# Kernel optimization log

Hardware: AMD Instinct MI355X
Metric: run time of the kernel (lower is better)

Reference implementation:

```python
import jax, jax.numpy as jnp
import numpy as np

NUM_HEADS = 4
NUM_GROUPS = 8
EPS = 1e-5


def group_norm(x, gamma, beta):
    # x: [b, c, h, w], GroupNorm with NUM_GROUPS groups, eps=1e-5
    b, c, h, w = x.shape
    xg = x.reshape(b, NUM_GROUPS, (c // NUM_GROUPS) * h * w)
    mean = jnp.mean(xg, axis=-1, keepdims=True)
    var = jnp.var(xg, axis=-1, keepdims=True)
    xn = ((xg - mean) * jax.lax.rsqrt(var + EPS)).reshape(b, c, h, w)
    return xn * gamma[None, :, None, None] + beta[None, :, None, None]


def setup_inputs() -> dict:
    key = jax.random.key(0)
    ks = jax.random.split(key, 4)
    b, c, h, w = 4, 256, 64, 64
    x = jax.random.normal(ks[0], (b, c, h, w), dtype=jnp.float32)
    gamma = jnp.ones((c,), dtype=jnp.float32)
    beta = jnp.zeros((c,), dtype=jnp.float32)
    w_qkv = jax.random.normal(ks[1], (3 * c, c), dtype=jnp.float32) * (c ** -0.5)
    b_qkv = jnp.zeros((3 * c,), dtype=jnp.float32)
    w_proj = jax.random.normal(ks[2], (c, c), dtype=jnp.float32) * (c ** -0.5)
    b_proj = jnp.zeros((c,), dtype=jnp.float32)
    return {"x": x, "gamma": gamma, "beta": beta, "w_qkv": w_qkv,
            "b_qkv": b_qkv, "w_proj": w_proj, "b_proj": b_proj}


def reference(x, gamma, beta, w_qkv, b_qkv, w_proj, b_proj):
    b, c, h, w = x.shape
    heads = NUM_HEADS
    dim = c // heads
    n = h * w
    residual = x
    xn = group_norm(x, gamma, beta)
    # 1x1 conv == per-pixel linear: [b,c,h,w] x [3c,c] -> [b,3c,h,w]
    qkv = jnp.einsum('bchw,oc->bohw', xn, w_qkv) + b_qkv[None, :, None, None]
    # channel layout: (three, heads, dim)
    qkv = qkv.reshape(b, 3, heads, dim, n)            # [b,3,H,D,N]
    qkv = jnp.transpose(qkv, (1, 0, 2, 4, 3))         # [3,b,H,N,D]
    q, k, v = qkv[0], qkv[1], qkv[2]
    scale = dim ** -0.5
    scores = jnp.einsum('bhid,bhjd->bhij', q * scale, k)  # [b,H,N,N]
    attn = jax.nn.softmax(scores, axis=-1)
    out = jnp.einsum('bhij,bhjd->bhid', attn, v)          # [b,H,N,D]
    out = jnp.transpose(out, (0, 1, 3, 2)).reshape(b, c, h, w)
    out = jnp.einsum('bchw,oc->bohw', out, w_proj) + b_proj[None, :, None, None]
    return out + residual
```

## Files before the change

### kernel.cpp

```cpp
#include <hip/hip_runtime.h>
#include <stdint.h>

typedef unsigned short ushort_t;
typedef __attribute__((ext_vector_type(8))) short bf16x8;
typedef __attribute__((ext_vector_type(4))) float f32x4;
typedef __attribute__((ext_vector_type(16))) float f32x16;
typedef __attribute__((ext_vector_type(4))) unsigned int u32x4;

__device__ __forceinline__ ushort_t f2bf(float f) {
  union { float f; unsigned u; } v; v.f = f;
  unsigned r = v.u + 0x7fffu + ((v.u >> 16) & 1u);
  return (ushort_t)(r >> 16);
}
__device__ __forceinline__ unsigned bfbits(float f) {
  union { float f; unsigned u; } v; v.f = f; return v.u;
}
__device__ __forceinline__ unsigned pack_trunc(float lo, float hi) {
#if __has_builtin(__builtin_amdgcn_perm)
  return __builtin_amdgcn_perm(bfbits(hi), bfbits(lo), 0x07060302u);
#else
  return (bfbits(lo) >> 16) | (bfbits(hi) & 0xffff0000u);
#endif
}
__device__ __forceinline__ unsigned pack_rn(float lo, float hi) {
  return (unsigned)f2bf(lo) | ((unsigned)f2bf(hi) << 16);
}
__device__ __forceinline__ void swap32(unsigned &a, unsigned &b) {
#if __has_builtin(__builtin_amdgcn_permlane32_swap)
  auto r = __builtin_amdgcn_permlane32_swap(a, b, false, false);
  a = r[0]; b = r[1];
#else
  asm volatile("v_permlane32_swap_b32 %0, %1" : "+v"(a), "+v"(b));
#endif
}
__device__ __forceinline__ float fast_exp2(float x) {
#if __has_builtin(__builtin_amdgcn_exp2f)
  return __builtin_amdgcn_exp2f(x);
#else
  float r; asm("v_exp_f32 %0, %1" : "=v"(r) : "v"(x)); return r;
#endif
}

#define SCALE_Q 0.18033688011112042f
#define EXP_BIAS 23.083109273961734f

__global__ __launch_bounds__(256)
void gn_stats1(const float* __restrict__ x, float2* __restrict__ partial) {
  int blk = blockIdx.x, tid = threadIdx.x;
  const float* base = x + (size_t)blk * 16384;
  float s = 0.f, ss = 0.f;
  for (int i = tid * 4; i < 16384; i += 1024) {
    float4 v = *(const float4*)(base + i);
    s  += v.x + v.y + v.z + v.w;
    ss += v.x*v.x + v.y*v.y + v.z*v.z + v.w*v.w;
  }
  __shared__ float rs[256], rss[256];
  rs[tid] = s; rss[tid] = ss;
  __syncthreads();
  for (int off = 128; off > 0; off >>= 1) {
    if (tid < off) { rs[tid] += rs[tid+off]; rss[tid] += rss[tid+off]; }
    __syncthreads();
  }
  if (tid == 0) partial[blk] = make_float2(rs[0], rss[0]);
}

__global__ __launch_bounds__(64)
void gn_stats2(const float2* __restrict__ partial, float* __restrict__ stats) {
  int g = threadIdx.x;
  if (g < 32) {
    float s = 0.f, ss = 0.f;
    #pragma unroll
    for (int k = 0; k < 8; k++) { float2 p = partial[g*8 + k]; s += p.x; ss += p.y; }
    float mean = s * (1.f/131072.f);
    float var  = ss * (1.f/131072.f) - mean*mean;
    stats[g*2]   = mean;
    stats[g*2+1] = rsqrtf(var + 1e-5f);
  }
}

__global__ __launch_bounds__(256)
void gn_apply_t(const float* __restrict__ x, const float* __restrict__ stats,
                const float* __restrict__ gamma, const float* __restrict__ beta,
                ushort_t* __restrict__ xn_t, int b0) {
  int blk = blockIdx.x;
  int tid = threadIdx.x;
  int ct = blk & 7;
  int nt = (blk >> 3) & 15;
  int bl = blk >> 7;
  int b  = b0 + bl;
  int c0 = ct * 32;
  float mean = stats[(b*8 + ct)*2];
  float rstd = stats[(b*8 + ct)*2 + 1];
  __shared__ ushort_t Ls[32][264];
  for (int idx = tid; idx < 32*64; idx += 256) {
    int cc = idx >> 6, seg = idx & 63;
    float ga = gamma[c0+cc], be = beta[c0+cc];
    float a = rstd * ga;
    float bb = be - mean * a;
    float4 v = *(const float4*)(x + ((size_t)(b*256 + c0 + cc))*4096 + nt*256 + seg*4);
    ushort4 t4 = make_ushort4(f2bf(v.x*a+bb), f2bf(v.y*a+bb), f2bf(v.z*a+bb), f2bf(v.w*a+bb));
    *(ushort4*)&Ls[cc][seg*4] = t4;
  }
  __syncthreads();
  for (int idx = tid; idx < 256*4; idx += 256) {
    int n = idx >> 2, seg = idx & 3;
    union { ushort_t u[8]; uint4 v; } pk;
    #pragma unroll
    for (int e = 0; e < 8; e++) pk.u[e] = Ls[seg*8 + e][n];
    *(uint4*)(xn_t + ((size_t)(bl*4096 + nt*256 + n))*256 + c0 + seg*8) = pk.v;
  }
}

__global__ __launch_bounds__(256)
void wconv2(const float* __restrict__ wq, const float* __restrict__ wp,
            ushort_t* __restrict__ oq, ushort_t* __restrict__ op) {
  int blk = blockIdx.x;
  const float* w; ushort_t* o; int i;
  if (blk < 192) { w = wq; o = oq; i = blk*256 + threadIdx.x; }
  else           { w = wp; o = op; i = (blk-192)*256 + threadIdx.x; }
  float4 v = *(const float4*)(w + (size_t)i*4);
  *(ushort4*)(o + (size_t)i*4) = make_ushort4(f2bf(v.x), f2bf(v.y), f2bf(v.z), f2bf(v.w));
}

__global__ __launch_bounds__(256)
void gemm_qkv(const ushort_t* __restrict__ A, const ushort_t* __restrict__ Bt,
              const float* __restrict__ bias, ushort_t* __restrict__ q,
              ushort_t* __restrict__ kbuf, ushort_t* __restrict__ vt, int b0) {
  int blk = blockIdx.x;
  int nt = blk % 12, mt = blk / 12;
  int m0 = mt*128, n0 = nt*64;
  int tid = threadIdx.x;
  int wave = tid >> 6, lane = tid & 63, quad = lane >> 4, l16 = lane & 15;
  __shared__ ushort_t As[128][40];
  __shared__ ushort_t Bs[64][40];
  __shared__ ushort_t Lt[64][136];
  f32x4 acc[2][4];
  #pragma unroll
  for (int i = 0; i < 2; i++)
    #pragma unroll
    for (int j = 0; j < 4; j++) acc[i][j] = (f32x4){0.f,0.f,0.f,0.f};

  for (int k0 = 0; k0 < 256; k0 += 32) {
    #pragma unroll
    for (int i = tid; i < 512; i += 256) {
      int row = i >> 2, seg = i & 3;
      *(uint4*)&As[row][seg*8] = *(const uint4*)(A + (size_t)(m0+row)*256 + k0 + seg*8);
    }
    {
      int row = tid >> 2, seg = tid & 3;
      *(uint4*)&Bs[row][seg*8] = *(const uint4*)(Bt + (size_t)(n0+row)*256 + k0 + seg*8);
    }
    __syncthreads();
    bf16x8 af[2], bfr[4];
    #pragma unroll
    for (int t = 0; t < 2; t++) af[t]  = *(const bf16x8*)&As[wave*32 + t*16 + l16][quad*8];
    #pragma unroll
    for (int t = 0; t < 4; t++) bfr[t] = *(const bf16x8*)&Bs[t*16 + l16][quad*8];
    #pragma unroll
    for (int ti = 0; ti < 2; ti++)
      #pragma unroll
      for (int jn = 0; jn < 4; jn++)
        acc[ti][jn] = __builtin_amdgcn_mfma_f32_16x16x32_bf16(af[ti], bfr[jn], acc[ti][jn], 0, 0, 0);
    __syncthreads();
  }

  int region = nt >> 2;
  if (region == 0) {
    #pragma unroll
    for (int jn = 0; jn < 4; jn++) {
      int n = n0 + jn*16 + l16;
      float bv = bias[n];
      #pragma unroll
      for (int ti = 0; ti < 2; ti++) {
        int mrow = m0 + wave*32 + ti*16 + quad*4;
        #pragma unroll
        for (int r = 0; r < 4; r++)
          q[(size_t)(b0*4096 + mrow + r)*256 + n] = f2bf((acc[ti][jn][r] + bv) * SCALE_Q);
      }
    }
  } else if (region == 1) {
    #pragma unroll
    for (int jn = 0; jn < 4; jn++) {
      int n = n0 + jn*16 + l16;
      float bv = bias[n];
      #pragma unroll
      for (int ti = 0; ti < 2; ti++) {
        int mrow = m0 + wave*32 + ti*16 + quad*4;
        #pragma unroll
        for (int r = 0; r < 4; r++)
          kbuf[(size_t)(b0*4096 + mrow + r)*256 + (n - 256)] = f2bf(acc[ti][jn][r] + bv);
      }
    }
  } else {
    int hh = nt - 8;
    int b_loc = m0 >> 12;
    #pragma unroll
    for (int jn = 0; jn < 4; jn++) {
      int n = n0 + jn*16 + l16;
      float bv = bias[n];
      int drow = jn*16 + l16;
      #pragma unroll
      for (int ti = 0; ti < 2; ti++) {
        int tcol = wave*32 + ti*16 + quad*4;
        uint2 w;
        w.x = pack_rn(acc[ti][jn][0] + bv, acc[ti][jn][1] + bv);
        w.y = pack_rn(acc[ti][jn][2] + bv, acc[ti][jn][3] + bv);
        *(uint2*)&Lt[drow][tcol] = w;
      }
    }
    __syncthreads();
    size_t vb_ = ((size_t)((b0 + b_loc)*4 + hh)*64)*4096 + (size_t)(m0 & 4095);
    for (int idx = tid; idx < 1024; idx += 256) {
      int dd = idx >> 4, toff = (idx & 15)*8;
      *(uint4*)(vt + vb_ + (size_t)dd*4096 + toff) = *(const uint4*)&Lt[dd][toff];
    }
  }
}

__global__ __launch_bounds__(256)
void attn(ushort_t* __restrict__ q, const ushort_t* __restrict__ k,
          const ushort_t* __restrict__ vt, int cpx) {
  int L = blockIdx.x;
  int blk = (L & 7) * cpx + (L >> 3);
  int it = blk & 31;
  int h  = (blk >> 5) & 3;
  int b  = blk >> 7;
  int i0 = it * 128;
  int tid = threadIdx.x;
  int wave = tid >> 6, lane = tid & 63;
  int q32 = lane & 31, hi = lane >> 5;

  __shared__ ushort_t Ks[2][64][72];
  __shared__ ushort_t Vs[2][64][72];

  const ushort_t* kbase = k + (size_t)(b*4096)*256 + h*64;
  const ushort_t* vbase = vt + (size_t)(b*4 + h)*64*4096;
  ushort_t* qrow = q + (size_t)(b*4096 + i0 + wave*32 + q32)*256 + h*64;

  bf16x8 qb0 = *(const bf16x8*)(qrow      + hi*8);
  bf16x8 qb1 = *(const bf16x8*)(qrow + 16 + hi*8);
  bf16x8 qb2 = *(const bf16x8*)(qrow + 32 + hi*8);
  bf16x8 qb3 = *(const bf16x8*)(qrow + 48 + hi*8);

  bf16x8 ones;
  #pragma unroll
  for (int e = 0; e < 8; e++) ones[e] = (short)0x3F80;

  f32x16 bias_init;
  #pragma unroll
  for (int r = 0; r < 16; r++) bias_init[r] = -EXP_BIAS;

  f32x16 o_acc0, o_acc1, l_acc;
  #pragma unroll
  for (int r = 0; r < 16; r++) { o_acc0[r] = 0.f; o_acc1[r] = 0.f; l_acc[r] = 0.f; }

  int srow = tid >> 2, scol = (tid & 3) * 16;
  const ushort_t* kp = kbase + (size_t)srow*256 + scol;
  const ushort_t* vp = vbase + (size_t)srow*4096 + scol;
  uint4 rk0, rk1, rv0, rv1;
  #define LOADK() { \
    rk0 = *(const uint4*)(kp); \
    rk1 = *(const uint4*)(kp + 8); \
    kp += 64*256; }
  #define WRITEK(BI) { \
    *(uint4*)&Ks[BI][srow][scol]     = rk0; \
    *(uint4*)&Ks[BI][srow][scol + 8] = rk1; }
  #define LOADV() { \
    rv0 = *(const uint4*)(vp); \
    rv1 = *(const uint4*)(vp + 8); \
    vp += 64; }
  #define WRITEV(BI) { \
    *(uint4*)&Vs[BI][srow][scol]     = rv0; \
    *(uint4*)&Vs[BI][srow][scol + 8] = rv1; }

  #define SOFTMAX(S, PB0, PB1) \
    _Pragma("unroll") \
    for (int r = 0; r < 16; r++) S[r] = fast_exp2(S[r]); \
    { unsigned pkA = pack_trunc(S[0],  S[1]),  pkB = pack_trunc(S[2],  S[3]); \
      unsigned pkC = pack_trunc(S[4],  S[5]),  pkD = pack_trunc(S[6],  S[7]); \
      unsigned pkE = pack_trunc(S[8],  S[9]),  pkF = pack_trunc(S[10], S[11]); \
      unsigned pkG = pack_trunc(S[12], S[13]), pkH = pack_trunc(S[14], S[15]); \
      swap32(pkA, pkC); swap32(pkB, pkD); \
      swap32(pkE, pkG); swap32(pkF, pkH); \
      u32x4 w0_ = {pkA, pkB, pkC, pkD}; \
      u32x4 w1_ = {pkE, pkF, pkG, pkH}; \
      PB0 = __builtin_bit_cast(bf16x8, w0_); \
      PB1 = __builtin_bit_cast(bf16x8, w1_); }

  #define WINDOW(BI) { \
    bf16x8 k00 = *(const bf16x8*)&Ks[BI][q32     ][hi*8]; \
    bf16x8 k01 = *(const bf16x8*)&Ks[BI][q32     ][16 + hi*8]; \
    bf16x8 k02 = *(const bf16x8*)&Ks[BI][q32     ][32 + hi*8]; \
    bf16x8 k03 = *(const bf16x8*)&Ks[BI][q32     ][48 + hi*8]; \
    bf16x8 k10 = *(const bf16x8*)&Ks[BI][32 + q32][hi*8]; \
    bf16x8 k11 = *(const bf16x8*)&Ks[BI][32 + q32][16 + hi*8]; \
    bf16x8 k12 = *(const bf16x8*)&Ks[BI][32 + q32][32 + hi*8]; \
    bf16x8 k13 = *(const bf16x8*)&Ks[BI][32 + q32][48 + hi*8]; \
    __builtin_amdgcn_s_setprio(1); \
    f32x16 s0 = __builtin_amdgcn_mfma_f32_32x32x16_bf16(k00, qb0, bias_init, 0, 0, 0); \
    s0 = __builtin_amdgcn_mfma_f32_32x32x16_bf16(k01, qb1, s0, 0, 0, 0); \
    s0 = __builtin_amdgcn_mfma_f32_32x32x16_bf16(k02, qb2, s0, 0, 0, 0); \
    s0 = __builtin_amdgcn_mfma_f32_32x32x16_bf16(k03, qb3, s0, 0, 0, 0); \
    f32x16 s1 = __builtin_amdgcn_mfma_f32_32x32x16_bf16(k10, qb0, bias_init, 0, 0, 0); \
    s1 = __builtin_amdgcn_mfma_f32_32x32x16_bf16(k11, qb1, s1, 0, 0, 0); \
    s1 = __builtin_amdgcn_mfma_f32_32x32x16_bf16(k12, qb2, s1, 0, 0, 0); \
    s1 = __builtin_amdgcn_mfma_f32_32x32x16_bf16(k13, qb3, s1, 0, 0, 0); \
    bf16x8 pb00, pb01, pb10, pb11; \
    SOFTMAX(s0, pb00, pb01)    \
    { bf16x8 vb00 = *(const bf16x8*)&Vs[BI][q32     ][hi*8]; \
      bf16x8 vb01 = *(const bf16x8*)&Vs[BI][q32     ][16 + hi*8]; \
      bf16x8 vb10 = *(const bf16x8*)&Vs[BI][32 + q32][hi*8]; \
      bf16x8 vb11 = *(const bf16x8*)&Vs[BI][32 + q32][16 + hi*8]; \
      o_acc0 = __builtin_amdgcn_mfma_f32_32x32x16_bf16(vb00, pb00, o_acc0, 0, 0, 0); \
      o_acc0 = __builtin_amdgcn_mfma_f32_32x32x16_bf16(vb01, pb01, o_acc0, 0, 0, 0); \
      o_acc1 = __builtin_amdgcn_mfma_f32_32x32x16_bf16(vb10, pb00, o_acc1, 0, 0, 0); \
      o_acc1 = __builtin_amdgcn_mfma_f32_32x32x16_bf16(vb11, pb01, o_acc1, 0, 0, 0); \
      l_acc  = __builtin_amdgcn_mfma_f32_32x32x16_bf16(ones, pb00, l_acc, 0, 0, 0); \
      l_acc  = __builtin_amdgcn_mfma_f32_32x32x16_bf16(ones, pb01, l_acc, 0, 0, 0); } \
    SOFTMAX(s1, pb10, pb11)    \
    { bf16x8 vb00 = *(const bf16x8*)&Vs[BI][q32     ][32 + hi*8]; \
      bf16x8 vb01 = *(const bf16x8*)&Vs[BI][q32     ][48 + hi*8]; \
      bf16x8 vb10 = *(const bf16x8*)&Vs[BI][32 + q32][32 + hi*8]; \
      bf16x8 vb11 = *(const bf16x8*)&Vs[BI][32 + q32][48 + hi*8]; \
      o_acc0 = __builtin_amdgcn_mfma_f32_32x32x16_bf16(vb00, pb10, o_acc0, 0, 0, 0); \
      o_acc0 = __builtin_amdgcn_mfma_f32_32x32x16_bf16(vb01, pb11, o_acc0, 0, 0, 0); \
      o_acc1 = __builtin_amdgcn_mfma_f32_32x32x16_bf16(vb10, pb10, o_acc1, 0, 0, 0); \
      o_acc1 = __builtin_amdgcn_mfma_f32_32x32x16_bf16(vb11, pb11, o_acc1, 0, 0, 0); \
      l_acc  = __builtin_amdgcn_mfma_f32_32x32x16_bf16(ones, pb10, l_acc, 0, 0, 0); \
      l_acc  = __builtin_amdgcn_mfma_f32_32x32x16_bf16(ones, pb11, l_acc, 0, 0, 0); } \
    __builtin_amdgcn_s_setprio(0); \
  }

  LOADK(); LOADV(); WRITEK(0); WRITEV(0);
  __syncthreads();

  #pragma unroll 2
  for (int w = 0; w < 64; w++) {
    int cur = w & 1;
    if (w < 63) { LOADK(); LOADV(); }
    WINDOW(cur)
    if (w < 63) { WRITEK(cur ^ 1); WRITEV(cur ^ 1); }
    __syncthreads();
  }
  #undef LOADK
  #undef LOADV
  #undef WRITEK
  #undef WRITEV
  #undef WINDOW
  #undef SOFTMAX

  float inv = 1.f / l_acc[0];

  #pragma unroll
  for (int g = 0; g < 4; g++) {
    ushort4 u;
    u.x = f2bf(o_acc0[g*4+0]*inv); u.y = f2bf(o_acc0[g*4+1]*inv);
    u.z = f2bf(o_acc0[g*4+2]*inv); u.w = f2bf(o_acc0[g*4+3]*inv);
    *(ushort4*)(qrow + g*8 + hi*4) = u;
  }
  #pragma unroll
  for (int g = 0; g < 4; g++) {
    ushort4 u;
    u.x = f2bf(o_acc1[g*4+0]*inv); u.y = f2bf(o_acc1[g*4+1]*inv);
    u.z = f2bf(o_acc1[g*4+2]*inv); u.w = f2bf(o_acc1[g*4+3]*inv);
    *(ushort4*)(qrow + 32 + g*8 + hi*4) = u;
  }
}

__global__ __launch_bounds__(256)
void gemm_proj(const ushort_t* __restrict__ A,
               const ushort_t* __restrict__ Bt,
               const float* __restrict__ bias, const float* __restrict__ resid,
               float* __restrict__ out, int col_base) {
  int blk = blockIdx.x;
  int mt = blk & 1, nt = blk >> 1;
  int m0 = mt*128, n0 = nt*64;
  int tid = threadIdx.x;
  int wave = tid >> 6, lane = tid & 63, quad = lane >> 4, l16 = lane & 15;
  __shared__ ushort_t As[128][40];
  __shared__ ushort_t Bs[64][40];
  f32x4 acc[2][4];
  #pragma unroll
  for (int i = 0; i < 2; i++)
    #pragma unroll
    for (int j = 0; j < 4; j++) acc[i][j] = (f32x4){0.f,0.f,0.f,0.f};

  for (int k0 = 0; k0 < 256; k0 += 32) {
    #pragma unroll
    for (int i = tid; i < 512; i += 256) {
      int row = i >> 2, seg = i & 3;
      *(uint4*)&As[row][seg*8] = *(const uint4*)(A + (size_t)(m0+row)*256 + k0 + seg*8);
    }
    {
      int row = tid >> 2, seg = tid & 3;
      *(uint4*)&Bs[row][seg*8] = *(const uint4*)(Bt + (size_t)(n0+row)*256 + k0 + seg*8);
    }
    __syncthreads();
    bf16x8 af[2], bfr[4];
    #pragma unroll
    for (int t = 0; t < 2; t++) af[t]  = *(const bf16x8*)&As[wave*32 + t*16 + l16][quad*8];
    #pragma unroll
    for (int t = 0; t < 4; t++) bfr[t] = *(const bf16x8*)&Bs[t*16 + l16][quad*8];
    #pragma unroll
    for (int ti = 0; ti < 2; ti++)
      #pragma unroll
      for (int jn = 0; jn < 4; jn++)
        acc[ti][jn] = __builtin_amdgcn_mfma_f32_16x16x32_bf16(af[ti], bfr[jn], acc[ti][jn], 0, 0, 0);
    __syncthreads();
  }
  #pragma unroll
  for (int jn = 0; jn < 4; jn++) {
    int col = col_base + n0 + jn*16 + l16;
    int bb = col >> 12;
    int np = col & 4095;
    #pragma unroll
    for (int ti = 0; ti < 2; ti++) {
      int o = m0 + wave*32 + ti*16 + quad*4;
      #pragma unroll
      for (int r = 0; r < 4; r++) {
        int oo = o + r;
        size_t addr = ((size_t)(bb*256 + oo))*4096 + np;
        out[addr] = acc[ti][jn][r] + bias[oo] + resid[addr];
      }
    }
  }
}

extern "C" void kernel_launch(void* const* d_in, const int* in_sizes, int n_in,
                              void* d_out, int out_size, void* d_ws, size_t ws_size,
                              hipStream_t stream) {
  const float* x      = (const float*)d_in[0];
  const float* gamma  = (const float*)d_in[1];
  const float* beta   = (const float*)d_in[2];
  const float* w_qkv  = (const float*)d_in[3];
  const float* b_qkv  = (const float*)d_in[4];
  const float* w_proj = (const float*)d_in[5];
  const float* b_proj = (const float*)d_in[6];
  float* out = (float*)d_out;

  char* ws = (char*)d_ws;
  float*  stats    = (float*)ws;
  float2* partial  = (float2*)(ws + 1024);
  ushort_t* wqkv_bf  = (ushort_t*)(ws + 4096);
  ushort_t* wproj_bf = (ushort_t*)(ws + 397312);
  char* big = ws + 528384;

  gn_stats1<<<dim3(256), dim3(256), 0, stream>>>(x, partial);
  gn_stats2<<<dim3(1), dim3(64), 0, stream>>>(partial, stats);
  wconv2<<<dim3(256), dim3(256), 0, stream>>>(w_qkv, w_proj, wqkv_bf, wproj_bf);

  if (ws_size >= (size_t)528384 + 3*(size_t)8388608 + (size_t)4194304) {
    ushort_t* q    = (ushort_t*)big;
    ushort_t* kbuf = (ushort_t*)(big + (size_t)8388608);
    ushort_t* vt   = (ushort_t*)(big + (size_t)16777216);
    ushort_t* xn   = (ushort_t*)(big + (size_t)25165824);
    for (int c = 0; c < 2; c++) {
      int b0 = c * 2;
      gn_apply_t<<<dim3(256), dim3(256), 0, stream>>>(x, stats, gamma, beta, xn, b0);
      gemm_qkv<<<dim3(768), dim3(256), 0, stream>>>(xn, wqkv_bf, b_qkv, q, kbuf, vt, b0);
    }
    attn<<<dim3(512), dim3(256), 0, stream>>>(q, kbuf, vt, 64);
    gemm_proj<<<dim3(512), dim3(256), 0, stream>>>(wproj_bf, q, b_proj, x, out, 0);
  } else {
    ushort_t* q_c  = (ushort_t*)big;
    ushort_t* k_c  = (ushort_t*)(big + (size_t)2097152);
    ushort_t* vt_c = (ushort_t*)(big + (size_t)4194304);
    ushort_t* xn_c = (ushort_t*)(big + (size_t)6291456);
    for (int b0 = 0; b0 < 4; b0++) {
      gn_apply_t<<<dim3(128), dim3(256), 0, stream>>>(x, stats, gamma, beta, xn_c, b0);
      gemm_qkv<<<dim3(384), dim3(256), 0, stream>>>(xn_c, wqkv_bf, b_qkv, q_c, k_c, vt_c, 0);
      attn<<<dim3(128), dim3(256), 0, stream>>>(q_c, k_c, vt_c, 16);
      gemm_proj<<<dim3(128), dim3(256), 0, stream>>>(wproj_bf, q_c, b_proj, x, out, b0*4096);
    }
  }
}
```

Before: 229.9 us.

## Fold GN stats finalize into apply, remap QKV GEMM blocks, hoist V loads

Removes the single-block gn_stats2 launch by having each gn_apply_t block reduce the 8 partial sums itself and compute mean/rstd. Remaps gemm_qkv block indices so consecutive blocks are spread across 8 groups (XCD-aware swizzle), aiming for better L2 locality per chiplet. In the attention window, V fragments are loaded from LDS before the score MFMAs and the setprio regions are narrowed around MFMA bursts to hide LDS latency. Costs slightly more redundant partial reads and extra register pressure for the early V loads.

```diff
diff --git a/kernel.cpp b/kernel.cpp
--- a/kernel.cpp
+++ b/kernel.cpp
@@ -64,22 +64,8 @@
   if (tid == 0) partial[blk] = make_float2(rs[0], rss[0]);
 }
 
-__global__ __launch_bounds__(64)
-void gn_stats2(const float2* __restrict__ partial, float* __restrict__ stats) {
-  int g = threadIdx.x;
-  if (g < 32) {
-    float s = 0.f, ss = 0.f;
-    #pragma unroll
-    for (int k = 0; k < 8; k++) { float2 p = partial[g*8 + k]; s += p.x; ss += p.y; }
-    float mean = s * (1.f/131072.f);
-    float var  = ss * (1.f/131072.f) - mean*mean;
-    stats[g*2]   = mean;
-    stats[g*2+1] = rsqrtf(var + 1e-5f);
-  }
-}
-
-__global__ __launch_bounds__(256)
-void gn_apply_t(const float* __restrict__ x, const float* __restrict__ stats,
+__global__ __launch_bounds__(256)
+void gn_apply_t(const float* __restrict__ x, const float2* __restrict__ partial,
                 const float* __restrict__ gamma, const float* __restrict__ beta,
                 ushort_t* __restrict__ xn_t, int b0) {
   int blk = blockIdx.x;
@@ -89,8 +75,14 @@
   int bl = blk >> 7;
   int b  = b0 + bl;
   int c0 = ct * 32;
-  float mean = stats[(b*8 + ct)*2];
-  float rstd = stats[(b*8 + ct)*2 + 1];
+  float s = 0.f, ss = 0.f;
+  #pragma unroll
+  for (int kk = 0; kk < 8; kk++) {
+    float2 p = partial[(b*8 + ct)*8 + kk];
+    s += p.x; ss += p.y;
+  }
+  float mean = s * (1.f/131072.f);
+  float rstd = rsqrtf(ss * (1.f/131072.f) - mean*mean + 1e-5f);
   __shared__ ushort_t Ls[32][264];
   for (int idx = tid; idx < 32*64; idx += 256) {
     int cc = idx >> 6, seg = idx & 63;
@@ -125,8 +117,10 @@
 __global__ __launch_bounds__(256)
 void gemm_qkv(const ushort_t* __restrict__ A, const ushort_t* __restrict__ Bt,
               const float* __restrict__ bias, ushort_t* __restrict__ q,
-              ushort_t* __restrict__ kbuf, ushort_t* __restrict__ vt, int b0) {
-  int blk = blockIdx.x;
+              ushort_t* __restrict__ kbuf, ushort_t* __restrict__ vt,
+              int b0, int cpx) {
+  int L = blockIdx.x;
+  int blk = (L & 7) * cpx + (L >> 3);
   int nt = blk % 12, mt = blk / 12;
   int m0 = mt*128, n0 = nt*64;
   int tid = threadIdx.x;
@@ -296,6 +290,10 @@
     bf16x8 k11 = *(const bf16x8*)&Ks[BI][32 + q32][16 + hi*8]; \
     bf16x8 k12 = *(const bf16x8*)&Ks[BI][32 + q32][32 + hi*8]; \
     bf16x8 k13 = *(const bf16x8*)&Ks[BI][32 + q32][48 + hi*8]; \
+    bf16x8 va00 = *(const bf16x8*)&Vs[BI][q32     ][hi*8]; \
+    bf16x8 va01 = *(const bf16x8*)&Vs[BI][q32     ][16 + hi*8]; \
+    bf16x8 va10 = *(const bf16x8*)&Vs[BI][32 + q32][hi*8]; \
+    bf16x8 va11 = *(const bf16x8*)&Vs[BI][32 + q32][16 + hi*8]; \
     __builtin_amdgcn_s_setprio(1); \
     f32x16 s0 = __builtin_amdgcn_mfma_f32_32x32x16_bf16(k00, qb0, bias_init, 0, 0, 0); \
     s0 = __builtin_amdgcn_mfma_f32_32x32x16_bf16(k01, qb1, s0, 0, 0, 0); \
@@ -305,29 +303,29 @@
     s1 = __builtin_amdgcn_mfma_f32_32x32x16_bf16(k11, qb1, s1, 0, 0, 0); \
     s1 = __builtin_amdgcn_mfma_f32_32x32x16_bf16(k12, qb2, s1, 0, 0, 0); \
     s1 = __builtin_amdgcn_mfma_f32_32x32x16_bf16(k13, qb3, s1, 0, 0, 0); \
+    __builtin_amdgcn_s_setprio(0); \
+    bf16x8 vc00 = *(const bf16x8*)&Vs[BI][q32     ][32 + hi*8]; \
+    bf16x8 vc01 = *(const bf16x8*)&Vs[BI][q32     ][48 + hi*8]; \
+    bf16x8 vc10 = *(const bf16x8*)&Vs[BI][32 + q32][32 + hi*8]; \
+    bf16x8 vc11 = *(const bf16x8*)&Vs[BI][32 + q32][48 + hi*8]; \
     bf16x8 pb00, pb01, pb10, pb11; \
     SOFTMAX(s0, pb00, pb01)    \
-    { bf16x8 vb00 = *(const bf16x8*)&Vs[BI][q32     ][hi*8]; \
-      bf16x8 vb01 = *(const bf16x8*)&Vs[BI][q32     ][16 + hi*8]; \
-      bf16x8 vb10 = *(const bf16x8*)&Vs[BI][32 + q32][hi*8]; \
-      bf16x8 vb11 = *(const bf16x8*)&Vs[BI][32 + q32][16 + hi*8]; \
-      o_acc0 = __builtin_amdgcn_mfma_f32_32x32x16_bf16(vb00, pb00, o_acc0, 0, 0, 0); \
-      o_acc0 = __builtin_amdgcn_mfma_f32_32x32x16_bf16(vb01, pb01, o_acc0, 0, 0, 0); \
-      o_acc1 = __builtin_amdgcn_mfma_f32_32x32x16_bf16(vb10, pb00, o_acc1, 0, 0, 0); \
-      o_acc1 = __builtin_amdgcn_mfma_f32_32x32x16_bf16(vb11, pb01, o_acc1, 0, 0, 0); \
-      l_acc  = __builtin_amdgcn_mfma_f32_32x32x16_bf16(ones, pb00, l_acc, 0, 0, 0); \
-      l_acc  = __builtin_amdgcn_mfma_f32_32x32x16_bf16(ones, pb01, l_acc, 0, 0, 0); } \
+    __builtin_amdgcn_s_setprio(1); \
+    o_acc0 = __builtin_amdgcn_mfma_f32_32x32x16_bf16(va00, pb00, o_acc0, 0, 0, 0); \
+    o_acc0 = __builtin_amdgcn_mfma_f32_32x32x16_bf16(va01, pb01, o_acc0, 0, 0, 0); \
+    o_acc1 = __builtin_amdgcn_mfma_f32_32x32x16_bf16(va10, pb00, o_acc1, 0, 0, 0); \
+    o_acc1 = __builtin_amdgcn_mfma_f32_32x32x16_bf16(va11, pb01, o_acc1, 0, 0, 0); \
+    l_acc  = __builtin_amdgcn_mfma_f32_32x32x16_bf16(ones, pb00, l_acc, 0, 0, 0); \
+    l_acc  = __builtin_amdgcn_mfma_f32_32x32x16_bf16(ones, pb01, l_acc, 0, 0, 0); \
+    __builtin_amdgcn_s_setprio(0); \
     SOFTMAX(s1, pb10, pb11)    \
-    { bf16x8 vb00 = *(const bf16x8*)&Vs[BI][q32     ][32 + hi*8]; \
-      bf16x8 vb01 = *(const bf16x8*)&Vs[BI][q32     ][48 + hi*8]; \
-      bf16x8 vb10 = *(const bf16x8*)&Vs[BI][32 + q32][32 + hi*8]; \
-      bf16x8 vb11 = *(const bf16x8*)&Vs[BI][32 + q32][48 + hi*8]; \
-      o_acc0 = __builtin_amdgcn_mfma_f32_32x32x16_bf16(vb00, pb10, o_acc0, 0, 0, 0); \
-      o_acc0 = __builtin_amdgcn_mfma_f32_32x32x16_bf16(vb01, pb11, o_acc0, 0, 0, 0); \
-      o_acc1 = __builtin_amdgcn_mfma_f32_32x32x16_bf16(vb10, pb10, o_acc1, 0, 0, 0); \
-      o_acc1 = __builtin_amdgcn_mfma_f32_32x32x16_bf16(vb11, pb11, o_acc1, 0, 0, 0); \
-      l_acc  = __builtin_amdgcn_mfma_f32_32x32x16_bf16(ones, pb10, l_acc, 0, 0, 0); \
-      l_acc  = __builtin_amdgcn_mfma_f32_32x32x16_bf16(ones, pb11, l_acc, 0, 0, 0); } \
+    __builtin_amdgcn_s_setprio(1); \
+    o_acc0 = __builtin_amdgcn_mfma_f32_32x32x16_bf16(vc00, pb10, o_acc0, 0, 0, 0); \
+    o_acc0 = __builtin_amdgcn_mfma_f32_32x32x16_bf16(vc01, pb11, o_acc0, 0, 0, 0); \
+    o_acc1 = __builtin_amdgcn_mfma_f32_32x32x16_bf16(vc10, pb10, o_acc1, 0, 0, 0); \
+    o_acc1 = __builtin_amdgcn_mfma_f32_32x32x16_bf16(vc11, pb11, o_acc1, 0, 0, 0); \
+    l_acc  = __builtin_amdgcn_mfma_f32_32x32x16_bf16(ones, pb10, l_acc, 0, 0, 0); \
+    l_acc  = __builtin_amdgcn_mfma_f32_32x32x16_bf16(ones, pb11, l_acc, 0, 0, 0); \
     __builtin_amdgcn_s_setprio(0); \
   }
 
@@ -439,14 +437,12 @@
   float* out = (float*)d_out;
 
   char* ws = (char*)d_ws;
-  float*  stats    = (float*)ws;
   float2* partial  = (float2*)(ws + 1024);
   ushort_t* wqkv_bf  = (ushort_t*)(ws + 4096);
   ushort_t* wproj_bf = (ushort_t*)(ws + 397312);
   char* big = ws + 528384;
 
   gn_stats1<<<dim3(256), dim3(256), 0, stream>>>(x, partial);
-  gn_stats2<<<dim3(1), dim3(64), 0, stream>>>(partial, stats);
   wconv2<<<dim3(256), dim3(256), 0, stream>>>(w_qkv, w_proj, wqkv_bf, wproj_bf);
 
   if (ws_size >= (size_t)528384 + 3*(size_t)8388608 + (size_t)4194304) {
@@ -456,8 +452,8 @@
     ushort_t* xn   = (ushort_t*)(big + (size_t)25165824);
     for (int c = 0; c < 2; c++) {
       int b0 = c * 2;
-      gn_apply_t<<<dim3(256), dim3(256), 0, stream>>>(x, stats, gamma, beta, xn, b0);
-      gemm_qkv<<<dim3(768), dim3(256), 0, stream>>>(xn, wqkv_bf, b_qkv, q, kbuf, vt, b0);
+      gn_apply_t<<<dim3(256), dim3(256), 0, stream>>>(x, partial, gamma, beta, xn, b0);
+      gemm_qkv<<<dim3(768), dim3(256), 0, stream>>>(xn, wqkv_bf, b_qkv, q, kbuf, vt, b0, 96);
     }
     attn<<<dim3(512), dim3(256), 0, stream>>>(q, kbuf, vt, 64);
     gemm_proj<<<dim3(512), dim3(256), 0, stream>>>(wproj_bf, q, b_proj, x, out, 0);
@@ -467,8 +463,8 @@
     ushort_t* vt_c = (ushort_t*)(big + (size_t)4194304);
     ushort_t* xn_c = (ushort_t*)(big + (size_t)6291456);
     for (int b0 = 0; b0 < 4; b0++) {
-      gn_apply_t<<<dim3(128), dim3(256), 0, stream>>>(x, stats, gamma, beta, xn_c, b0);
-      gemm_qkv<<<dim3(384), dim3(256), 0, stream>>>(xn_c, wqkv_bf, b_qkv, q_c, k_c, vt_c, 0);
+      gn_apply_t<<<dim3(128), dim3(256), 0, stream>>>(x, partial, gamma, beta, xn_c, b0);
+      gemm_qkv<<<dim3(384), dim3(256), 0, stream>>>(xn_c, wqkv_bf, b_qkv, q_c, k_c, vt_c, 0, 48);
       attn<<<dim3(128), dim3(256), 0, stream>>>(q_c, k_c, vt_c, 16);
       gemm_proj<<<dim3(128), dim3(256), 0, stream>>>(wproj_bf, q_c, b_proj, x, out, b0*4096);
     }
```

Result: faster. 222.1 us (-3.4%).
